# Optimization experiments

Hardware: AMD Instinct MI355X
Metric: run time of the kernel (lower is better)

The kernel has to match this reference:

```python
import jax, jax.numpy as jnp
import numpy as np

HIDDEN = 4096
N_HEADS = 32
HEAD_DIM = HIDDEN // N_HEADS  # 128
ROPE_BASE = 10000.0


def _rotate_half(x):
    h = x.shape[-1] // 2
    return jnp.concatenate((-x[..., h:], x[..., :h]), axis=-1)


def _rope_sin_cos(position_ids):
    # position_ids: [B, S] int -> sin, cos: [B, 1, S, head_dim]
    inv_freq = 1.0 / (ROPE_BASE ** (jnp.arange(0, HEAD_DIM, 2, dtype=jnp.float32) / HEAD_DIM))
    freqs = position_ids.astype(jnp.float32)[..., None] * inv_freq  # [B,S,hd/2]
    emb = jnp.concatenate((freqs, freqs), axis=-1)  # [B,S,hd]
    return jnp.sin(emb)[:, None, :, :], jnp.cos(emb)[:, None, :, :]


def setup_inputs() -> dict:
    key = jax.random.key(0)
    k1, k2, k3 = jax.random.split(key, 3)
    B, S = 2, 2048
    hidden_states = jax.random.normal(k1, (B, S, HIDDEN), dtype=jnp.float32)
    w_qkv = jax.random.normal(k2, (HIDDEN, 3 * HIDDEN), dtype=jnp.float32) * 0.02
    wo = jax.random.normal(k3, (HIDDEN, HIDDEN), dtype=jnp.float32) * 0.02
    position_ids = jnp.broadcast_to(jnp.arange(S, dtype=jnp.int32)[None, :], (B, S))
    return {"hidden_states": hidden_states, "w_qkv": w_qkv, "wo": wo,
            "position_ids": position_ids}


def reference(hidden_states, w_qkv, wo, position_ids):
    B, S, H = hidden_states.shape
    qkv = hidden_states @ w_qkv  # [B,S,3H]
    q, k, v = jnp.split(qkv, 3, axis=-1)
    # [B,S,nH,hd] -> [B,nH,S,hd]
    q = q.reshape(B, S, N_HEADS, HEAD_DIM).transpose(0, 2, 1, 3)
    k = k.reshape(B, S, N_HEADS, HEAD_DIM).transpose(0, 2, 1, 3)
    v = v.reshape(B, S, N_HEADS, HEAD_DIM).transpose(0, 2, 1, 3)
    sin, cos = _rope_sin_cos(position_ids)  # [B,1,S,hd]
    q = q * cos + _rotate_half(q) * sin
    k = k * cos + _rotate_half(k) * sin
    scale = 1.0 / np.sqrt(HEAD_DIM)
    scores = jnp.einsum('bhqd,bhkd->bhqk', q, k) * scale
    causal = jnp.tril(jnp.ones((S, S), dtype=bool))
    scores = jnp.where(causal[None, None, :, :], scores, jnp.finfo(scores.dtype).min)
    attn = jax.nn.softmax(scores, axis=-1)
    out = jnp.einsum('bhqk,bhkd->bhqd', attn, v)  # [B,nH,S,hd]
    out = out.transpose(0, 2, 1, 3).reshape(B, S, H)
    return out @ wo
```

## Files before the change

### kernel.cpp

```cpp
#include <hip/hip_runtime.h>

typedef unsigned int u32;
typedef unsigned short u16;
typedef short short8 __attribute__((ext_vector_type(8)));
typedef float f32x4 __attribute__((ext_vector_type(4)));
typedef unsigned short us4 __attribute__((ext_vector_type(4)));

#define S_LEN 2048
#define BATCH 2
#define HID 4096
#define NH 32
#define HD 128
#define TRIH 12288

#define GCAST(p) ((const __attribute__((address_space(1))) u32*)(p))
#define LCAST(p) ((__attribute__((address_space(3))) u32*)(p))

static __device__ __forceinline__ u16 f2bf(float f) {
  union { float f; u32 u; } x; x.f = f;
  u32 u = x.u;
  u32 r = u + 0x7FFFu + ((u >> 16) & 1u);
  return (u16)(r >> 16);
}
static __device__ __forceinline__ float bf2f(u16 h) {
  union { u32 u; float f; } x; x.u = ((u32)h) << 16;
  return x.f;
}

__global__ __launch_bounds__(256) void cvt_f32_bf16(const float* __restrict__ in,
                                                    u16* __restrict__ out, int n4) {
  int i = blockIdx.x * 256 + threadIdx.x;
  if (i >= n4) return;
  float4 v = ((const float4*)in)[i];
  us4 o;
  o.x = f2bf(v.x); o.y = f2bf(v.y); o.z = f2bf(v.z); o.w = f2bf(v.w);
  ((us4*)out)[i] = o;
}

__global__ __launch_bounds__(256) void tr_cvt(const float* __restrict__ in,
                                              u16* __restrict__ out, int R, int C) {
  __shared__ float tile[64][65];
  int c0 = blockIdx.x * 64, r0 = blockIdx.y * 64;
  int tx = threadIdx.x;
  int rr = tx >> 4;
  int cc = (tx & 15) << 2;
#pragma unroll
  for (int it = 0; it < 4; ++it) {
    float4 v = *(const float4*)&in[(size_t)(r0 + rr + it * 16) * C + c0 + cc];
    tile[rr + it * 16][cc + 0] = v.x;
    tile[rr + it * 16][cc + 1] = v.y;
    tile[rr + it * 16][cc + 2] = v.z;
    tile[rr + it * 16][cc + 3] = v.w;
  }
  __syncthreads();
#pragma unroll
  for (int it = 0; it < 4; ++it) {
    int crow = rr + it * 16;
    us4 o;
    o.x = f2bf(tile[cc + 0][crow]);
    o.y = f2bf(tile[cc + 1][crow]);
    o.z = f2bf(tile[cc + 2][crow]);
    o.w = f2bf(tile[cc + 3][crow]);
    *(us4*)&out[(size_t)(c0 + crow) * R + r0 + cc] = o;
  }
}


template<int MQ, int NQ>
static __device__ __forceinline__ void mfma_quad(f32x4 (&acc)[8][4], short8 (&af)[4][2],
                                                 short8 (&bfr)[4][2]) {
#pragma unroll
  for (int ml = 0; ml < 4; ++ml)
#pragma unroll
    for (int nl = 0; nl < 2; ++nl) {
      acc[MQ*4+ml][NQ*2+nl] = __builtin_amdgcn_mfma_f32_16x16x32_bf16(
          af[ml][0], bfr[NQ*2+nl][0], acc[MQ*4+ml][NQ*2+nl], 0, 0, 0);
      acc[MQ*4+ml][NQ*2+nl] = __builtin_amdgcn_mfma_f32_16x16x32_bf16(
          af[ml][1], bfr[NQ*2+nl][1], acc[MQ*4+ml][NQ*2+nl], 0, 0, 0);
    }
}

template<int MQ>
static __device__ __forceinline__ void read_a(short8 (&af)[4][2], const u16* abase, int lane) {
#pragma unroll
  for (int ml = 0; ml < 4; ++ml) {
    int r = MQ*64 + ml*16 + (lane & 15);
#pragma unroll
    for (int kh = 0; kh < 2; ++kh) {
      int j = kh*4 + (lane >> 4);
      af[ml][kh] = *(const short8*)(abase + r*64 + ((j ^ (r & 7)) << 3));
    }
  }
}
template<int NQ>
static __device__ __forceinline__ void read_b(short8 (&bfr)[4][2], const u16* bbase,
                                              int rbase, int lane) {
#pragma unroll
  for (int nl = 0; nl < 2; ++nl) {
    int r = rbase + (NQ*2+nl)*16 + (lane & 15);
#pragma unroll
    for (int kh = 0; kh < 2; ++kh) {
      int j = kh*4 + (lane >> 4);
      bfr[NQ*2+nl][kh] = *(const short8*)(bbase + r*64 + ((j ^ (r & 7)) << 3));
    }
  }
}

#define PHASE_CLOSE() \
  __builtin_amdgcn_s_barrier(); \
  __builtin_amdgcn_sched_barrier(0);

#define SEAM_CLOSE(NSTR) \
  asm volatile("s_waitcnt vmcnt(" NSTR ")" ::: "memory"); \
  __builtin_amdgcn_s_barrier(); \
  __builtin_amdgcn_sched_barrier(0);

template<int OUTF32>
__global__ __launch_bounds__(512, 1) void gemm256(const u16* __restrict__ A,
                                                  const u16* __restrict__ Bt,
                                                  void* __restrict__ Cout,
                                                  int M, int N, int K, int nbm) {
  __shared__ __attribute__((aligned(16))) u16 lds[65536];
  const int tid = threadIdx.x, wave = tid >> 6, lane = tid & 63;
  const int wr = wave >> 2, wc = wave & 3;
  const int nwg = gridDim.x, wg = blockIdx.x, cpx = nwg >> 3;
  const int swz = (wg & 7) * cpx + (wg >> 3);
  const size_t tileM = (size_t)(swz % nbm) * 256;
  const size_t tileN = (size_t)(swz / nbm) * 256;
  const int nIter = K >> 7;

  const int r_ = tid >> 3;
  const int gc_ = (tid & 7) ^ (r_ & 7);

  const u16* Ag = A + tileM * K;
  const u16* Bg = Bt + tileN * K;

  f32x4 acc[8][4] = {};
  short8 af[4][2], bfr[4][2];

  auto stageA = [&](int kt, int buf, int half) {
    const u16* g0 = Ag + (size_t)(half*128 + r_) * K + kt*64 + (gc_ << 3);
    u16* l = lds + buf*16384 + half*8192 + wave*512;
    __builtin_amdgcn_global_load_lds(GCAST(g0), LCAST(l), 16, 0, 0);
    __builtin_amdgcn_global_load_lds(GCAST(g0 + (size_t)64*K), LCAST(l + 4096), 16, 0, 0);
  };
  auto stageB = [&](int kt, int buf, int half) {
    const u16* g0 = Bg + (size_t)(half*128 + r_) * K + kt*64 + (gc_ << 3);
    u16* l = lds + 32768 + buf*16384 + half*8192 + wave*512;
    __builtin_amdgcn_global_load_lds(GCAST(g0), LCAST(l), 16, 0, 0);
    __builtin_amdgcn_global_load_lds(GCAST(g0 + (size_t)64*K), LCAST(l + 4096), 16, 0, 0);
  };

  const u16* a0 = lds + wr*8192;
  const u16* a1 = lds + 16384 + wr*8192;
  const u16* b0 = lds + 32768 + (wc >> 1)*8192;
  const u16* b1 = lds + 32768 + 16384 + (wc >> 1)*8192;
  const int brb = (wc & 1) * 64;

  stageA(0, 0, 0); stageA(0, 0, 1);
  stageB(0, 0, 0); stageB(0, 0, 1);
  stageB(1, 1, 0); stageB(1, 1, 1);
  SEAM_CLOSE("4")

  for (int i = 0; i < nIter; ++i) {
    const int t1 = 2*i + 1, t2 = 2*i + 2, t3 = 2*i + 3;
    const bool more = (i + 1 < nIter);

    read_a<0>(af, a0, lane);
    read_b<0>(bfr, b0, brb, lane);
    read_b<1>(bfr, b0, brb, lane);
    stageA(t1, 1, 0); stageA(t1, 1, 1);
    __builtin_amdgcn_s_setprio(1);
    mfma_quad<0, 0>(acc, af, bfr);
    mfma_quad<0, 1>(acc, af, bfr);
    __builtin_amdgcn_s_setprio(0);
    PHASE_CLOSE()

    read_a<1>(af, a0, lane);
    if (more) { stageB(t2, 0, 0); stageB(t2, 0, 1); }
    __builtin_amdgcn_s_setprio(1);
    mfma_quad<1, 0>(acc, af, bfr);
    mfma_quad<1, 1>(acc, af, bfr);
    __builtin_amdgcn_s_setprio(0);
    if (more) { SEAM_CLOSE("4") } else { SEAM_CLOSE("0") }

    read_a<0>(af, a1, lane);
    read_b<0>(bfr, b1, brb, lane);
    read_b<1>(bfr, b1, brb, lane);
    if (more) { stageA(t2, 0, 0); stageA(t2, 0, 1); }
    __builtin_amdgcn_s_setprio(1);
    mfma_quad<0, 0>(acc, af, bfr);
    mfma_quad<0, 1>(acc, af, bfr);
    __builtin_amdgcn_s_setprio(0);
    PHASE_CLOSE()

    read_a<1>(af, a1, lane);
    if (more) { stageB(t3, 1, 0); stageB(t3, 1, 1); }
    __builtin_amdgcn_s_setprio(1);
    mfma_quad<1, 0>(acc, af, bfr);
    mfma_quad<1, 1>(acc, af, bfr);
    __builtin_amdgcn_s_setprio(0);
    if (more) { SEAM_CLOSE("4") } else { PHASE_CLOSE() }
  }

  const int r0o = (lane >> 4) << 2, c0o = lane & 15;
#pragma unroll
  for (int m = 0; m < 8; ++m)
#pragma unroll
    for (int n = 0; n < 4; ++n)
#pragma unroll
      for (int rr = 0; rr < 4; ++rr) {
        size_t grow = tileM + wr*128 + m*16 + r0o + rr;
        size_t gcol = tileN + wc*64 + n*16 + c0o;
        if (OUTF32) ((float*)Cout)[grow * N + gcol] = acc[m][n][rr];
        else        ((u16*)Cout)[grow * N + gcol] = f2bf(acc[m][n][rr]);
      }
}

__global__ __launch_bounds__(256) void rope_kernel(u16* __restrict__ qkv,
                                                   const int* __restrict__ pid) {
  int idx = blockIdx.x * 256 + threadIdx.x;
  int row = idx >> 9;
  int rem = idx & 511;
  int which = rem >> 8;
  int h = (rem >> 3) & 31;
  int j0 = (rem & 7) << 3;
  u16* p = qkv + (size_t)row * TRIH + which * HID + h * HD + j0;
  short8 lo = *(short8*)p;
  short8 hi = *(short8*)(p + 64);
  float pos = (float)pid[row];
  short8 olo, ohi;
#pragma unroll
  for (int i = 0; i < 8; ++i) {
    float x0 = bf2f((u16)lo[i]), x1 = bf2f((u16)hi[i]);
    float th = pos * expf(-(float)(j0 + i) * 0.14391156831212787f);
    float sn, cs;
    sincosf(th, &sn, &cs);
    olo[i] = (short)f2bf(x0 * cs - x1 * sn);
    ohi[i] = (short)f2bf(x1 * cs + x0 * sn);
  }
  *(short8*)p = olo;
  *(short8*)(p + 64) = ohi;
}

__global__ __launch_bounds__(512, 2) void attn_kernel(const u16* __restrict__ qkv,
                                                      u16* __restrict__ O) {
  const int bid = blockIdx.x;
  const int qt = 15 - (bid >> 6);
  const int bh = bid & 63;
  const int b = bh >> 5, h = bh & 31;
  const int tid = threadIdx.x, wave = tid >> 6, lane = tid & 63;
  __shared__ u16 Ks[2][64 * 128];
  __shared__ u16 VsT[2][128 * 64];
  __shared__ u16 Ps[8][16 * 64];
  const u16* base = qkv + (size_t)b * S_LEN * TRIH + h * HD;

  const int rbase = (lane >> 4) << 2;
  const int cbase = lane & 15;
  const int q_lo = qt * 128;
  const int wrow0 = q_lo + wave * 16;

  short8 qf[4];
  {
    const u16* qrow = base + (size_t)(wrow0 + cbase) * TRIH;
#pragma unroll
    for (int f = 0; f < 4; ++f)
      qf[f] = *(const short8*)(qrow + ((f * 4 + (lane >> 4)) << 3));
  }

  const int tmax_w = 2 * qt + (wave >= 4 ? 1 : 0);
  const int tmax_b = 2 * qt + 1;

  float mrun = -1e30f, lrun = 0.f;
  f32x4 accO[8] = {};

  short8 kreg[2], vreg[2];
  auto load_tile = [&](int t) {
    int kv = t << 6;
#pragma unroll
    for (int it = 0; it < 2; ++it) {
      int c = tid + it * 512;
      int row = c >> 4, ch = c & 15;
      const u16* src = base + (size_t)(kv + row) * TRIH + (ch << 3);
      kreg[it] = *(const short8*)(src + HID);
      vreg[it] = *(const short8*)(src + 2 * HID);
    }
  };
  auto write_tile = [&](int buf) {
#pragma unroll
    for (int it = 0; it < 2; ++it) {
      int c = tid + it * 512;
      int row = c >> 4, ch = c & 15;
      *(short8*)(Ks[buf] + row * 128 + ((ch ^ (row & 7)) << 3)) = kreg[it];
#pragma unroll
      for (int i = 0; i < 8; ++i) {
        int d = (ch << 3) + i;
        VsT[buf][d * 64 + (((row >> 3) ^ (ch & 7)) << 3) + (row & 7)] = (u16)vreg[it][i];
      }
    }
  };

  load_tile(0);
  write_tile(0);
  load_tile(1);

  for (int t = 0; t <= tmax_b; ++t) {
    const int cur = t & 1;
    __syncthreads();
    if (t < tmax_b) write_tile(cur ^ 1);
    if (t + 2 <= tmax_b) load_tile(t + 2);

    if (t > tmax_w) continue;

    f32x4 s[4] = {};
    __builtin_amdgcn_s_setprio(1);
#pragma unroll
    for (int n = 0; n < 4; ++n) {
      int krow = n * 16 + cbase;
#pragma unroll
      for (int f = 0; f < 4; ++f) {
        int ch = f * 4 + (lane >> 4);
        short8 kf = *(const short8*)(Ks[cur] + krow * 128 + ((ch ^ (krow & 7)) << 3));
        s[n] = __builtin_amdgcn_mfma_f32_16x16x32_bf16(kf, qf[f], s[n], 0, 0, 0);
      }
    }
    __builtin_amdgcn_s_setprio(0);
    const float scale = 0.08838834764831845f;
    const int kv0 = t << 6;
    const int qcol = wrow0 + cbase;
    if (t == tmax_w) {
#pragma unroll
      for (int n = 0; n < 4; ++n)
#pragma unroll
        for (int r = 0; r < 4; ++r) {
          int kvrow = kv0 + n * 16 + rbase + r;
          s[n][r] = (kvrow <= qcol) ? s[n][r] * scale : -1e30f;
        }
    } else {
#pragma unroll
      for (int n = 0; n < 4; ++n) s[n] *= scale;
    }

    float pmax = -1e30f;
#pragma unroll
    for (int n = 0; n < 4; ++n)
#pragma unroll
      for (int r = 0; r < 4; ++r) pmax = fmaxf(pmax, s[n][r]);
    pmax = fmaxf(pmax, __shfl_xor(pmax, 16));
    pmax = fmaxf(pmax, __shfl_xor(pmax, 32));

    if (__any(pmax > mrun + 8.0f)) {
      float mnew = fmaxf(mrun, pmax);
      float corr = __expf(mrun - mnew);
      float rs = 0.f;
#pragma unroll
      for (int n = 0; n < 4; ++n)
#pragma unroll
        for (int r = 0; r < 4; ++r) { float pv = __expf(s[n][r] - mnew); s[n][r] = pv; rs += pv; }
      rs += __shfl_xor(rs, 16); rs += __shfl_xor(rs, 32);
      lrun = lrun * corr + rs;
      mrun = mnew;
      float cq[4];
#pragma unroll
      for (int r = 0; r < 4; ++r) cq[r] = __shfl(corr, rbase + r);
#pragma unroll
      for (int nd = 0; nd < 8; ++nd)
#pragma unroll
        for (int r = 0; r < 4; ++r) accO[nd][r] *= cq[r];
    } else {
      float rs = 0.f;
#pragma unroll
      for (int n = 0; n < 4; ++n)
#pragma unroll
        for (int r = 0; r < 4; ++r) { float pv = __expf(s[n][r] - mrun); s[n][r] = pv; rs += pv; }
      rs += __shfl_xor(rs, 16); rs += __shfl_xor(rs, 32);
      lrun += rs;
    }

    u16* Pw = (u16*)Ps[wave];
#pragma unroll
    for (int n = 0; n < 4; ++n)
#pragma unroll
      for (int r = 0; r < 4; ++r) {
        int kv = n * 16 + rbase + r;
        Pw[cbase * 64 + (((kv >> 3) ^ (cbase & 7)) << 3) + (kv & 7)] = f2bf(s[n][r]);
      }

    short8 pa[2];
    {
      int prow = lane & 15;
#pragma unroll
      for (int f2 = 0; f2 < 2; ++f2) {
        int ch = f2 * 4 + (lane >> 4);
        pa[f2] = *(const short8*)(Pw + prow * 64 + ((ch ^ (prow & 7)) << 3));
      }
    }
    __builtin_amdgcn_s_setprio(1);
#pragma unroll
    for (int nd = 0; nd < 8; ++nd) {
      int drow = nd * 16 + cbase;
#pragma unroll
      for (int f2 = 0; f2 < 2; ++f2) {
        int ch = f2 * 4 + (lane >> 4);
        short8 vb = *(const short8*)(VsT[cur] + drow * 64 + ((ch ^ ((drow >> 3) & 7)) << 3));
        accO[nd] = __builtin_amdgcn_mfma_f32_16x16x32_bf16(pa[f2], vb, accO[nd], 0, 0, 0);
      }
    }
    __builtin_amdgcn_s_setprio(0);
  }

  float lq[4];
#pragma unroll
  for (int r = 0; r < 4; ++r) lq[r] = __shfl(lrun, rbase + r);
#pragma unroll
  for (int nd = 0; nd < 8; ++nd)
#pragma unroll
    for (int r = 0; r < 4; ++r) {
      int qrow = wrow0 + rbase + r;
      int col = h * HD + nd * 16 + cbase;
      O[(size_t)(b * S_LEN + qrow) * HID + col] = f2bf(accO[nd][r] / lq[r]);
    }
}

extern "C" void kernel_launch(void* const* d_in, const int* in_sizes, int n_in,
                              void* d_out, int out_size, void* d_ws, size_t ws_size,
                              hipStream_t stream) {
  const float* hidden = (const float*)d_in[0];
  const float* w_qkv  = (const float*)d_in[1];
  const float* wo     = (const float*)d_in[2];
  const int*   pid    = (const int*)d_in[3];

  const size_t MB = 1024ull * 1024ull;
  u16* hb    = (u16*)d_ws;
  u16* wqkvT = (u16*)((char*)d_ws + 32 * MB);
  u16* woT   = (u16*)((char*)d_ws + 128 * MB);
  u16* qkvb  = (u16*)((char*)d_ws + 160 * MB);
  u16* Obuf  = hb;

  cvt_f32_bf16<<<16384, 256, 0, stream>>>(hidden, hb, (BATCH * S_LEN * HID) / 4);
  tr_cvt<<<dim3(TRIH / 64, HID / 64), 256, 0, stream>>>(w_qkv, wqkvT, HID, TRIH);
  tr_cvt<<<dim3(HID / 64, HID / 64), 256, 0, stream>>>(wo, woT, HID, HID);

  gemm256<0><<<768, 512, 0, stream>>>(hb, wqkvT, qkvb, BATCH * S_LEN, TRIH, HID, 16);

  rope_kernel<<<(BATCH * S_LEN * 2 * NH * 8) / 256, 256, 0, stream>>>(qkvb, pid);

  attn_kernel<<<1024, 512, 0, stream>>>(qkvb, Obuf);

  gemm256<1><<<256, 512, 0, stream>>>(Obuf, woT, d_out, BATCH * S_LEN, HID, HID, 16);
}
```

Before: 725.6 us.

## Process two 16-row query sub-tiles per wave in attention with 4-wave blocks

The attention kernel now uses 256 threads (4 waves) per block, and each wave handles 32 query rows as two 16-row sub-tiles instead of 16 rows. Each K fragment and V fragment read from shared memory feeds two MFMAs, halving LDS reads per unit of compute and raising the MFMA-to-load ratio. The cost is doubled accumulator and softmax state per wave, which raises register pressure and may lower occupancy. The wave-level causal split also gets coarser, since each wave now covers 32 rows.

```diff
diff --git a/kernel.cpp b/kernel.cpp
--- a/kernel.cpp
+++ b/kernel.cpp
@@ -243,7 +243,7 @@
   *(short8*)(p + 64) = ohi;
 }
 
-__global__ __launch_bounds__(512, 2) void attn_kernel(const u16* __restrict__ qkv,
+__global__ __launch_bounds__(256, 2) void attn_kernel(const u16* __restrict__ qkv,
                                                       u16* __restrict__ O) {
   const int bid = blockIdx.x;
   const int qt = 15 - (bid >> 6);
@@ -252,34 +252,37 @@
   const int tid = threadIdx.x, wave = tid >> 6, lane = tid & 63;
   __shared__ u16 Ks[2][64 * 128];
   __shared__ u16 VsT[2][128 * 64];
-  __shared__ u16 Ps[8][16 * 64];
+  __shared__ u16 Ps[4][2][16 * 64];
   const u16* base = qkv + (size_t)b * S_LEN * TRIH + h * HD;
 
   const int rbase = (lane >> 4) << 2;
   const int cbase = lane & 15;
-  const int q_lo = qt * 128;
-  const int wrow0 = q_lo + wave * 16;
-
-  short8 qf[4];
+  const int wrow0 = qt * 128 + wave * 32;
+
+  short8 qf0[4], qf1[4];
   {
-    const u16* qrow = base + (size_t)(wrow0 + cbase) * TRIH;
-#pragma unroll
-    for (int f = 0; f < 4; ++f)
-      qf[f] = *(const short8*)(qrow + ((f * 4 + (lane >> 4)) << 3));
-  }
-
-  const int tmax_w = 2 * qt + (wave >= 4 ? 1 : 0);
+    const u16* q0 = base + (size_t)(wrow0 + cbase) * TRIH;
+    const u16* q1 = base + (size_t)(wrow0 + 16 + cbase) * TRIH;
+#pragma unroll
+    for (int f = 0; f < 4; ++f) {
+      int off = (f * 4 + (lane >> 4)) << 3;
+      qf0[f] = *(const short8*)(q0 + off);
+      qf1[f] = *(const short8*)(q1 + off);
+    }
+  }
+
+  const int tmax_w = 2 * qt + (wave >= 2 ? 1 : 0);
   const int tmax_b = 2 * qt + 1;
 
-  float mrun = -1e30f, lrun = 0.f;
-  f32x4 accO[8] = {};
-
-  short8 kreg[2], vreg[2];
+  float mrun0 = -1e30f, lrun0 = 0.f, mrun1 = -1e30f, lrun1 = 0.f;
+  f32x4 accO0[8] = {}, accO1[8] = {};
+
+  short8 kreg[4], vreg[4];
   auto load_tile = [&](int t) {
     int kv = t << 6;
 #pragma unroll
-    for (int it = 0; it < 2; ++it) {
-      int c = tid + it * 512;
+    for (int it = 0; it < 4; ++it) {
+      int c = tid + it * 256;
       int row = c >> 4, ch = c & 15;
       const u16* src = base + (size_t)(kv + row) * TRIH + (ch << 3);
       kreg[it] = *(const short8*)(src + HID);
@@ -288,8 +291,8 @@
   };
   auto write_tile = [&](int buf) {
 #pragma unroll
-    for (int it = 0; it < 2; ++it) {
-      int c = tid + it * 512;
+    for (int it = 0; it < 4; ++it) {
+      int c = tid + it * 256;
       int row = c >> 4, ch = c & 15;
       *(short8*)(Ks[buf] + row * 128 + ((ch ^ (row & 7)) << 3)) = kreg[it];
 #pragma unroll
@@ -312,7 +315,7 @@
 
     if (t > tmax_w) continue;
 
-    f32x4 s[4] = {};
+    f32x4 s0[4] = {}, s1[4] = {};
     __builtin_amdgcn_s_setprio(1);
 #pragma unroll
     for (int n = 0; n < 4; ++n) {
@@ -321,78 +324,105 @@
       for (int f = 0; f < 4; ++f) {
         int ch = f * 4 + (lane >> 4);
         short8 kf = *(const short8*)(Ks[cur] + krow * 128 + ((ch ^ (krow & 7)) << 3));
-        s[n] = __builtin_amdgcn_mfma_f32_16x16x32_bf16(kf, qf[f], s[n], 0, 0, 0);
+        s0[n] = __builtin_amdgcn_mfma_f32_16x16x32_bf16(kf, qf0[f], s0[n], 0, 0, 0);
+        s1[n] = __builtin_amdgcn_mfma_f32_16x16x32_bf16(kf, qf1[f], s1[n], 0, 0, 0);
       }
     }
     __builtin_amdgcn_s_setprio(0);
     const float scale = 0.08838834764831845f;
     const int kv0 = t << 6;
-    const int qcol = wrow0 + cbase;
     if (t == tmax_w) {
+      int qc0 = wrow0 + cbase, qc1 = wrow0 + 16 + cbase;
 #pragma unroll
       for (int n = 0; n < 4; ++n)
 #pragma unroll
         for (int r = 0; r < 4; ++r) {
           int kvrow = kv0 + n * 16 + rbase + r;
-          s[n][r] = (kvrow <= qcol) ? s[n][r] * scale : -1e30f;
+          s0[n][r] = (kvrow <= qc0) ? s0[n][r] * scale : -1e30f;
+          s1[n][r] = (kvrow <= qc1) ? s1[n][r] * scale : -1e30f;
         }
     } else {
 #pragma unroll
-      for (int n = 0; n < 4; ++n) s[n] *= scale;
-    }
-
-    float pmax = -1e30f;
+      for (int n = 0; n < 4; ++n) { s0[n] *= scale; s1[n] *= scale; }
+    }
+
+    float pmax0 = -1e30f, pmax1 = -1e30f;
 #pragma unroll
     for (int n = 0; n < 4; ++n)
 #pragma unroll
-      for (int r = 0; r < 4; ++r) pmax = fmaxf(pmax, s[n][r]);
-    pmax = fmaxf(pmax, __shfl_xor(pmax, 16));
-    pmax = fmaxf(pmax, __shfl_xor(pmax, 32));
-
-    if (__any(pmax > mrun + 8.0f)) {
-      float mnew = fmaxf(mrun, pmax);
-      float corr = __expf(mrun - mnew);
-      float rs = 0.f;
+      for (int r = 0; r < 4; ++r) {
+        pmax0 = fmaxf(pmax0, s0[n][r]);
+        pmax1 = fmaxf(pmax1, s1[n][r]);
+      }
+    pmax0 = fmaxf(pmax0, __shfl_xor(pmax0, 16));
+    pmax0 = fmaxf(pmax0, __shfl_xor(pmax0, 32));
+    pmax1 = fmaxf(pmax1, __shfl_xor(pmax1, 16));
+    pmax1 = fmaxf(pmax1, __shfl_xor(pmax1, 32));
+
+    bool need = (pmax0 > mrun0 + 8.0f) || (pmax1 > mrun1 + 8.0f);
+    if (__any(need)) {
+      float mn0 = fmaxf(mrun0, pmax0), mn1 = fmaxf(mrun1, pmax1);
+      float c0 = __expf(mrun0 - mn0), c1 = __expf(mrun1 - mn1);
+      float rs0 = 0.f, rs1 = 0.f;
 #pragma unroll
       for (int n = 0; n < 4; ++n)
 #pragma unroll
-        for (int r = 0; r < 4; ++r) { float pv = __expf(s[n][r] - mnew); s[n][r] = pv; rs += pv; }
-      rs += __shfl_xor(rs, 16); rs += __shfl_xor(rs, 32);
-      lrun = lrun * corr + rs;
-      mrun = mnew;
-      float cq[4];
-#pragma unroll
-      for (int r = 0; r < 4; ++r) cq[r] = __shfl(corr, rbase + r);
+        for (int r = 0; r < 4; ++r) {
+          float p0 = __expf(s0[n][r] - mn0); s0[n][r] = p0; rs0 += p0;
+          float p1 = __expf(s1[n][r] - mn1); s1[n][r] = p1; rs1 += p1;
+        }
+      rs0 += __shfl_xor(rs0, 16); rs0 += __shfl_xor(rs0, 32);
+      rs1 += __shfl_xor(rs1, 16); rs1 += __shfl_xor(rs1, 32);
+      lrun0 = lrun0 * c0 + rs0; mrun0 = mn0;
+      lrun1 = lrun1 * c1 + rs1; mrun1 = mn1;
+      float cq0[4], cq1[4];
+#pragma unroll
+      for (int r = 0; r < 4; ++r) {
+        cq0[r] = __shfl(c0, rbase + r);
+        cq1[r] = __shfl(c1, rbase + r);
+      }
 #pragma unroll
       for (int nd = 0; nd < 8; ++nd)
 #pragma unroll
-        for (int r = 0; r < 4; ++r) accO[nd][r] *= cq[r];
+        for (int r = 0; r < 4; ++r) {
+          accO0[nd][r] *= cq0[r];
+          accO1[nd][r] *= cq1[r];
+        }
     } else {
-      float rs = 0.f;
+      float rs0 = 0.f, rs1 = 0.f;
 #pragma unroll
       for (int n = 0; n < 4; ++n)
 #pragma unroll
-        for (int r = 0; r < 4; ++r) { float pv = __expf(s[n][r] - mrun); s[n][r] = pv; rs += pv; }
-      rs += __shfl_xor(rs, 16); rs += __shfl_xor(rs, 32);
-      lrun += rs;
-    }
-
-    u16* Pw = (u16*)Ps[wave];
+        for (int r = 0; r < 4; ++r) {
+          float p0 = __expf(s0[n][r] - mrun0); s0[n][r] = p0; rs0 += p0;
+          float p1 = __expf(s1[n][r] - mrun1); s1[n][r] = p1; rs1 += p1;
+        }
+      rs0 += __shfl_xor(rs0, 16); rs0 += __shfl_xor(rs0, 32);
+      rs1 += __shfl_xor(rs1, 16); rs1 += __shfl_xor(rs1, 32);
+      lrun0 += rs0; lrun1 += rs1;
+    }
+
+    u16* Pw0 = (u16*)Ps[wave][0];
+    u16* Pw1 = (u16*)Ps[wave][1];
 #pragma unroll
     for (int n = 0; n < 4; ++n)
 #pragma unroll
       for (int r = 0; r < 4; ++r) {
         int kv = n * 16 + rbase + r;
-        Pw[cbase * 64 + (((kv >> 3) ^ (cbase & 7)) << 3) + (kv & 7)] = f2bf(s[n][r]);
-      }
-
-    short8 pa[2];
+        int off = cbase * 64 + (((kv >> 3) ^ (cbase & 7)) << 3) + (kv & 7);
+        Pw0[off] = f2bf(s0[n][r]);
+        Pw1[off] = f2bf(s1[n][r]);
+      }
+
+    short8 pa0[2], pa1[2];
     {
       int prow = lane & 15;
 #pragma unroll
       for (int f2 = 0; f2 < 2; ++f2) {
         int ch = f2 * 4 + (lane >> 4);
-        pa[f2] = *(const short8*)(Pw + prow * 64 + ((ch ^ (prow & 7)) << 3));
+        int off = prow * 64 + ((ch ^ (prow & 7)) << 3);
+        pa0[f2] = *(const short8*)(Pw0 + off);
+        pa1[f2] = *(const short8*)(Pw1 + off);
       }
     }
     __builtin_amdgcn_s_setprio(1);
@@ -403,22 +433,28 @@
       for (int f2 = 0; f2 < 2; ++f2) {
         int ch = f2 * 4 + (lane >> 4);
         short8 vb = *(const short8*)(VsT[cur] + drow * 64 + ((ch ^ ((drow >> 3) & 7)) << 3));
-        accO[nd] = __builtin_amdgcn_mfma_f32_16x16x32_bf16(pa[f2], vb, accO[nd], 0, 0, 0);
-      }
-    }
-    __builtin_amdgcn_s_setprio(0);
-  }
-
-  float lq[4];
-#pragma unroll
-  for (int r = 0; r < 4; ++r) lq[r] = __shfl(lrun, rbase + r);
+        accO0[nd] = __builtin_amdgcn_mfma_f32_16x16x32_bf16(pa0[f2], vb, accO0[nd], 0, 0, 0);
+        accO1[nd] = __builtin_amdgcn_mfma_f32_16x16x32_bf16(pa1[f2], vb, accO1[nd], 0, 0, 0);
+      }
+    }
+    __builtin_amdgcn_s_setprio(0);
+  }
+
+  float lq0[4], lq1[4];
+#pragma unroll
+  for (int r = 0; r < 4; ++r) {
+    lq0[r] = __shfl(lrun0, rbase + r);
+    lq1[r] = __shfl(lrun1, rbase + r);
+  }
 #pragma unroll
   for (int nd = 0; nd < 8; ++nd)
 #pragma unroll
     for (int r = 0; r < 4; ++r) {
-      int qrow = wrow0 + rbase + r;
       int col = h * HD + nd * 16 + cbase;
-      O[(size_t)(b * S_LEN + qrow) * HID + col] = f2bf(accO[nd][r] / lq[r]);
+      int q0 = wrow0 + rbase + r;
+      int q1 = wrow0 + 16 + rbase + r;
+      O[(size_t)(b * S_LEN + q0) * HID + col] = f2bf(accO0[nd][r] / lq0[r]);
+      O[(size_t)(b * S_LEN + q1) * HID + col] = f2bf(accO1[nd][r] / lq1[r]);
     }
 }
 
@@ -445,7 +481,7 @@
 
   rope_kernel<<<(BATCH * S_LEN * 2 * NH * 8) / 256, 256, 0, stream>>>(qkvb, pid);
 
-  attn_kernel<<<1024, 512, 0, stream>>>(qkvb, Obuf);
+  attn_kernel<<<1024, 256, 0, stream>>>(qkvb, Obuf);
 
   gemm256<1><<<256, 512, 0, stream>>>(Obuf, woT, d_out, BATCH * S_LEN, HID, HID, 16);
 }
```

Measured after the change: 1.014 ms. 1.4x slower.
